# Optimization experiments

Measured on AMD Instinct MI355X. Metric: run time of the kernel, lower is better.

The kernel has to match this reference:

```python
import jax, jax.numpy as jnp
import numpy as np

THRESH = 0.3
DECAY = 0.5


def spike_fn(x):
    # Heaviside threshold (forward only)
    return (x > THRESH).astype(x.dtype)


def setup_inputs() -> dict:
    key = jax.random.key(0)
    k_in, k0, k1, k2 = jax.random.split(key, 4)
    B, D0, T = 128, 512, 512
    inputs = jax.random.uniform(k_in, (B, D0, T), dtype=jnp.float32)
    w0 = jax.random.normal(k0, (512, 1024), dtype=jnp.float32)
    w1 = jax.random.normal(k1, (1024, 1024), dtype=jnp.float32)
    w2 = jax.random.normal(k2, (1024, 512), dtype=jnp.float32)
    return {"inputs": inputs, "w0": w0, "w1": w1, "w2": w2}


def reference(inputs, w0, w1, w2):
    ws = (w0, w1, w2)
    B = inputs.shape[0]
    layer_dims = tuple(w.shape[1] for w in ws)

    # time-major: [T, B, D0]
    xs = jnp.transpose(inputs, (2, 0, 1))

    mem0 = tuple(jnp.zeros((B, d), dtype=inputs.dtype) for d in layer_dims)
    spk0 = tuple(jnp.zeros((B, d), dtype=inputs.dtype) for d in layer_dims)

    def step(carry, x_t):
        mems, spikes = carry
        prev_spike = x_t  # layer-0 spikes come straight from the input
        new_mems, new_spikes = [], []
        for i, w in enumerate(ws):
            # leaky integrate with reset-by-spike, then fire
            mem = mems[i] * DECAY * (1.0 - spikes[i]) + prev_spike @ w
            s = spike_fn(mem)
            new_mems.append(mem)
            new_spikes.append(s)
            prev_spike = s
        return (tuple(new_mems), tuple(new_spikes)), None

    (_, spikes_final), _ = jax.lax.scan(step, (mem0, spk0), xs)
    return spikes_final[-1]
```

## Files before the change

kernel.cpp:

```cpp
#include <hip/hip_runtime.h>


typedef __bf16 bf16;
typedef __attribute__((ext_vector_type(8))) __bf16 bf16x8;
typedef __attribute__((ext_vector_type(16))) float f32x16;
typedef unsigned long long u64;

#define B_   128
#define D0_  512
#define T_   512
#define TS_  128
#define N1_  1024
#define N2_  1024
#define N3_  512
#define MFMA32(a,b,c) __builtin_amdgcn_mfma_f32_32x32x16_bf16((a),(b),(c),0,0,0)

#define GL2LDS(g, l) __builtin_amdgcn_global_load_lds( \
    (const __attribute__((address_space(1))) void*)(g), \
    (__attribute__((address_space(3))) void*)(l), 16, 0, 0)

#define WAIT_BARRIER() do { \
    asm volatile("s_waitcnt vmcnt(0)" ::: "memory"); \
    __builtin_amdgcn_s_barrier(); } while (0)


__global__ __launch_bounds__(256)
void split_w(const float* __restrict__ W, bf16* __restrict__ WTh, bf16* __restrict__ WTl,
             int K, int N)
{
    __shared__ float tile[32][33];
    const int k0 = blockIdx.x * 32, n0 = blockIdx.y * 32;
    const int tx = threadIdx.x & 31, ty = threadIdx.x >> 5;
#pragma unroll
    for (int r = 0; r < 4; ++r)
        tile[ty + r * 8][tx] = W[(size_t)(k0 + ty + r * 8) * N + n0 + tx];
    __syncthreads();
#pragma unroll
    for (int r = 0; r < 4; ++r) {
        int nl = ty + r * 8;
        float v = tile[tx][nl];
        bf16 h = (bf16)v;
        size_t o = (size_t)(n0 + nl) * K + k0 + tx;
        WTh[o] = h;
        WTl[o] = (bf16)(v - (float)h);
    }
}

__global__ __launch_bounds__(64)
void split_wf(const float* __restrict__ W, bf16* __restrict__ Fh, bf16* __restrict__ Fl,
              int K, int N)
{
    const int l = threadIdx.x;
    const int kc = blockIdx.x;
    const int np = blockIdx.y;
    const int c  = np * 32 + (l & 31);
    const int k0 = kc * 16 + (l >> 5) * 8;
    const size_t ob = (((size_t)np * (K / 16) + kc) * 64 + l) * 8;
#pragma unroll
    for (int e = 0; e < 8; ++e) {
        float v = W[(size_t)(k0 + e) * N + c];
        bf16 h = (bf16)v;
        Fh[ob + e] = h;
        Fl[ob + e] = (bf16)(v - (float)h);
    }
}

__global__ __launch_bounds__(256)
void split_x(const float* __restrict__ in, bf16* __restrict__ Xh, bf16* __restrict__ Xl)
{
    __shared__ float tile[32][33];
    const int b = blockIdx.z, d0 = blockIdx.x * 32, t0 = blockIdx.y * 32;
    const int tx = threadIdx.x & 31, ty = threadIdx.x >> 5;
#pragma unroll
    for (int r = 0; r < 4; ++r)
        tile[ty + r * 8][tx] = in[((size_t)b * D0_ + d0 + ty + r * 8) * T_ + t0 + tx];
    __syncthreads();
    const int s = t0 >> 7;
#pragma unroll
    for (int r = 0; r < 4; ++r) {
        int t  = t0 + ty + r * 8;
        int tl = t & (TS_ - 1);
        float v = tile[tx][ty + r * 8];
        bf16 h = (bf16)v;
        size_t o = (((size_t)s * B_ + b) * TS_ + tl) * D0_ + d0 + tx;
        Xh[o] = h;
        Xl[o] = (bf16)(v - (float)h);
    }
}

__device__ __forceinline__ bf16x8 expand8(unsigned v)
{
    union { unsigned u[4]; bf16x8 h; } r;
    const unsigned p = v * 0x8001u;
#pragma unroll
    for (int i = 0; i < 4; ++i)
        r.u[i] = ((p >> (2 * i)) & 0x10001u) * 0x3F80u;
    return r.h;
}

__global__ __launch_bounds__(256, 2)
void snn_layer0(const bf16* __restrict__ Ah, const bf16* __restrict__ Al,
                const bf16* __restrict__ WTh, const bf16* __restrict__ WTl,
                u64* __restrict__ bitsOut)
{
    constexpr int K = D0_;
    __shared__ char smem[65536];
    bf16* sA0  = (bf16*)(smem);
    bf16* sAl0 = (bf16*)(smem + 8192);
    bf16* sB0  = (bf16*)(smem + 16384);
    bf16* sBl0 = (bf16*)(smem + 24576);
    bf16* sA1  = (bf16*)(smem + 32768);
    bf16* sAl1 = (bf16*)(smem + 40960);
    bf16* sB1  = (bf16*)(smem + 49152);
    bf16* sBl1 = (bf16*)(smem + 57344);
    float* If  = (float*)smem;

    const int tid = threadIdx.x, lane = tid & 63, w = tid >> 6;
    const int wm = w & 1, wn = w >> 1;
    const int l31 = lane & 31, kh = lane >> 5;
    const int bid = blockIdx.x;
    const int b  = (bid & 7) | ((bid >> 6) << 3);
    const int nb = ((bid >> 3) & 7) * 128;

    const int i4 = lane >> 2, c4 = lane & 3;
    const int csrc = c4 ^ ((i4 >> 1) & 3);
    const bf16* gBh = WTh + (size_t)(nb + w * 32 + i4) * K + csrc * 8;
    const bf16* gBl = WTl + (size_t)(nb + w * 32 + i4) * K + csrc * 8;
    const int wT = w * 32 * 32;

    int rA[2], rB[2], swA[2], swB[2];
#pragma unroll
    for (int i = 0; i < 2; ++i) {
        rA[i] = wm * 64 + i * 32 + l31;
        rB[i] = wn * 64 + i * 32 + l31;
        swA[i] = (rA[i] >> 1) & 3;
        swB[i] = (rB[i] >> 1) & 3;
    }

    float cm = 0.f, cs = 0.f;
    const int scol = tid & 63;
    float* Ifb = If + (tid >> 6) * 4096;

#define STAGE0(dA, dAl, dBh, dBl, go)                                          \
    do {                                                                       \
        _Pragma("unroll")                                                      \
        for (int inst = 0; inst < 2; ++inst) {                                 \
            GL2LDS(gA  + (size_t)(inst * 16) * K + (go), (dA)  + wT + inst * 16 * 32); \
            GL2LDS(gAl + (size_t)(inst * 16) * K + (go), (dAl) + wT + inst * 16 * 32); \
            GL2LDS(gBh + (size_t)(inst * 16) * K + (go), (dBh) + wT + inst * 16 * 32); \
            GL2LDS(gBl + (size_t)(inst * 16) * K + (go), (dBl) + wT + inst * 16 * 32); \
        }                                                                      \
    } while (0)

#define KSTEP0(cA, cAl, cBh, cBl)                                              \
    do {                                                                       \
        bf16x8 a[2][2], al2[2][2];                                             \
        _Pragma("unroll")                                                      \
        for (int mi = 0; mi < 2; ++mi)                                         \
            _Pragma("unroll")                                                  \
            for (int h = 0; h < 2; ++h) {                                      \
                const int off = rA[mi] * 32 + (((2 * h + kh) ^ swA[mi]) * 8);  \
                a[mi][h]   = *(const bf16x8*)((cA) + off);                     \
                al2[mi][h] = *(const bf16x8*)((cAl) + off);                    \
            }                                                                  \
        _Pragma("unroll")                                                      \
        for (int h = 0; h < 2; ++h) {                                          \
            bf16x8 bh[2], bl[2];                                               \
            _Pragma("unroll")                                                  \
            for (int ni = 0; ni < 2; ++ni) {                                   \
                const int off = rB[ni] * 32 + (((2 * h + kh) ^ swB[ni]) * 8);  \
                bh[ni] = *(const bf16x8*)((cBh) + off);                        \
                bl[ni] = *(const bf16x8*)((cBl) + off);                        \
            }                                                                  \
            _Pragma("unroll")                                                  \
            for (int ni = 0; ni < 2; ++ni)                                     \
                _Pragma("unroll")                                              \
                for (int mi = 0; mi < 2; ++mi)                                 \
                    acc[mi][ni] = MFMA32(a[mi][h], bh[ni], acc[mi][ni]);       \
            _Pragma("unroll")                                                  \
            for (int ni = 0; ni < 2; ++ni)                                     \
                _Pragma("unroll")                                              \
                for (int mi = 0; mi < 2; ++mi)                                 \
                    acc[mi][ni] = MFMA32(al2[mi][h], bh[ni], acc[mi][ni]);     \
            _Pragma("unroll")                                                  \
            for (int ni = 0; ni < 2; ++ni)                                     \
                _Pragma("unroll")                                              \
                for (int mi = 0; mi < 2; ++mi)                                 \
                    acc[mi][ni] = MFMA32(a[mi][h], bl[ni], acc[mi][ni]);       \
        }                                                                      \
        WAIT_BARRIER();                                                        \
    } while (0)

#pragma unroll 1
    for (int s = 0; s < T_ / TS_; ++s) {
        const size_t arow = ((size_t)s * B_ + b) * TS_;
        const bf16* gA  = Ah + (arow + w * 32 + i4) * K + csrc * 8;
        const bf16* gAl = Al + (arow + w * 32 + i4) * K + csrc * 8;

        STAGE0(sA0, sAl0, sB0, sBl0, 0);
        WAIT_BARRIER();

        f32x16 acc[2][2] = {};

#pragma unroll 1
        for (int ks = 0; ks < K / 32; ks += 2) {
            STAGE0(sA1, sAl1, sB1, sBl1, (ks + 1) * 32);
            KSTEP0(sA0, sAl0, sB0, sBl0);
            if (ks + 2 < K / 32)
                STAGE0(sA0, sAl0, sB0, sBl0, (ks + 2) * 32);
            KSTEP0(sA1, sAl1, sB1, sBl1);
        }

        u64 word0 = 0, word1 = 0;
        if (wm == 0) {
#pragma unroll
            for (int ni = 0; ni < 2; ++ni)
#pragma unroll
                for (int mi = 0; mi < 2; ++mi)
#pragma unroll
                    for (int r = 0; r < 16; ++r) {
                        const int tt = mi * 32 + (r & 3) + 8 * (r >> 2) + 4 * kh;
                        If[wn * 4096 + tt * 64 + ni * 32 + l31] = acc[mi][ni][r];
                    }
        }
        __syncthreads();
        if (tid < 128) {
            float m = cm, sp = cs;
#pragma unroll 4
            for (int tt = 0; tt < 64; ++tt) {
                m = m * 0.5f * (1.0f - sp) + Ifb[tt * 64 + scol];
                const bool fire = m > 0.3f;
                sp = fire ? 1.0f : 0.0f;
                u64 bal = __ballot(fire);
                if ((tid & 63) == tt) word0 = bal;
            }
            cm = m; cs = sp;
        }
        __syncthreads();
        if (wm == 1) {
#pragma unroll
            for (int ni = 0; ni < 2; ++ni)
#pragma unroll
                for (int mi = 0; mi < 2; ++mi)
#pragma unroll
                    for (int r = 0; r < 16; ++r) {
                        const int tt = mi * 32 + (r & 3) + 8 * (r >> 2) + 4 * kh;
                        If[wn * 4096 + tt * 64 + ni * 32 + l31] = acc[mi][ni][r];
                    }
        }
        __syncthreads();
        if (tid < 128) {
            float m = cm, sp = cs;
#pragma unroll 4
            for (int tt = 0; tt < 64; ++tt) {
                m = m * 0.5f * (1.0f - sp) + Ifb[tt * 64 + scol];
                const bool fire = m > 0.3f;
                sp = fire ? 1.0f : 0.0f;
                u64 bal = __ballot(fire);
                if ((tid & 63) == tt) word1 = bal;
            }
            cm = m; cs = sp;
            u64* dst = bitsOut + ((size_t)s * B_ + b) * 2048;
            const int j8 = (nb >> 6) + (tid >> 6);
            const int t0 = tid & 63, t1 = 64 + (tid & 63);
            dst[t0 * 16 + (j8 ^ (t0 & 15))] = word0;
            dst[t1 * 16 + (j8 ^ (t1 & 15))] = word1;
        }
        __syncthreads();
    }
#undef STAGE0
#undef KSTEP0
}

template<bool WRITE_BITS>
__global__ __launch_bounds__(256, 2)
void snn_layer_bits(const u64* __restrict__ bitsIn,
                    const bf16* __restrict__ WFh, const bf16* __restrict__ WFl,
                    u64* __restrict__ bitsOut, float* __restrict__ outp, int N)
{
    constexpr int K = 1024, KC = K / 16;
    __shared__ char smem[81920];
    char* bitsLds = smem;
    float* If = (float*)(smem + 16384);

    const int tid = threadIdx.x, lane = tid & 63, w = tid >> 6;
    const int l31 = lane & 31, kh = lane >> 5;
    const int b = blockIdx.y;
    const int nb = blockIdx.x * 128;

    const bf16* wfh = WFh + ((size_t)((nb >> 5) + w) * KC) * 512 + lane * 8;
    const bf16* wfl = WFl + ((size_t)((nb >> 5) + w) * KC) * 512 + lane * 8;

    const int sh8 = 8 * kh;
    const int s15 = l31 & 15;
    int rbase[4];
#pragma unroll
    for (int mi = 0; mi < 4; ++mi)
        rbase[mi] = (mi * 32 + l31) * 128;

    float cm = 0.f, cs = 0.f;

#define CPAIR(cb0, cb1, cb2, cb3)                                              \
    do {                                                                       \
        _Pragma("unroll")                                                      \
        for (int st = 0; st < 2; ++st) {                                       \
            _Pragma("unroll")                                                  \
            for (int h = 0; h < 2; ++h) {                                      \
                const int j = st * 2 + h;                                      \
                bf16x8 a0 = expand8((unsigned)((cb0) >> (32 * st + 16 * h + sh8)) & 0xFFu); \
                bf16x8 a1 = expand8((unsigned)((cb1) >> (32 * st + 16 * h + sh8)) & 0xFFu); \
                bf16x8 a2 = expand8((unsigned)((cb2) >> (32 * st + 16 * h + sh8)) & 0xFFu); \
                bf16x8 a3 = expand8((unsigned)((cb3) >> (32 * st + 16 * h + sh8)) & 0xFFu); \
                __builtin_amdgcn_s_setprio(1);                                 \
                acc[0] = MFMA32(a0, ch[j], acc[0]);                            \
                acc[1] = MFMA32(a1, ch[j], acc[1]);                            \
                acc[2] = MFMA32(a2, ch[j], acc[2]);                            \
                acc[3] = MFMA32(a3, ch[j], acc[3]);                            \
                acc[0] = MFMA32(a0, cl[j], acc[0]);                            \
                acc[1] = MFMA32(a1, cl[j], acc[1]);                            \
                acc[2] = MFMA32(a2, cl[j], acc[2]);                            \
                acc[3] = MFMA32(a3, cl[j], acc[3]);                            \
                __builtin_amdgcn_s_setprio(0);                                 \
            }                                                                  \
        }                                                                      \
    } while (0)

#pragma unroll 1
    for (int s = 0; s < T_ / TS_; ++s) {
        {
            const char* src = (const char*)bitsIn + ((size_t)s * B_ + b) * 16384;
#pragma unroll
            for (int i = 0; i < 4; ++i)
                GL2LDS(src + (w * 4 + i) * 1024 + lane * 16,
                       bitsLds + (w * 4 + i) * 1024);
        }
        WAIT_BARRIER();

        f32x16 acc[4] = {};

        u64 cb0, cb1, cb2, cb3;
        bf16x8 ch[4], cl[4];
        cb0 = *(const u64*)(bitsLds + rbase[0] + ((0 ^ s15) << 3));
        cb1 = *(const u64*)(bitsLds + rbase[1] + ((0 ^ s15) << 3));
        cb2 = *(const u64*)(bitsLds + rbase[2] + ((0 ^ s15) << 3));
        cb3 = *(const u64*)(bitsLds + rbase[3] + ((0 ^ s15) << 3));
#pragma unroll
        for (int j = 0; j < 4; ++j) {
            ch[j] = *(const bf16x8*)(wfh + (size_t)j * 512);
            cl[j] = *(const bf16x8*)(wfl + (size_t)j * 512);
        }

#pragma unroll 1
        for (int pi = 0; pi < 15; ++pi) {
            u64 nb0, nb1, nb2, nb3;
            bf16x8 nh[4], nl[4];
            nb0 = *(const u64*)(bitsLds + rbase[0] + (((pi + 1) ^ s15) << 3));
            nb1 = *(const u64*)(bitsLds + rbase[1] + (((pi + 1) ^ s15) << 3));
            nb2 = *(const u64*)(bitsLds + rbase[2] + (((pi + 1) ^ s15) << 3));
            nb3 = *(const u64*)(bitsLds + rbase[3] + (((pi + 1) ^ s15) << 3));
#pragma unroll
            for (int j = 0; j < 4; ++j) {
                nh[j] = *(const bf16x8*)(wfh + (size_t)((pi + 1) * 4 + j) * 512);
                nl[j] = *(const bf16x8*)(wfl + (size_t)((pi + 1) * 4 + j) * 512);
            }
            CPAIR(cb0, cb1, cb2, cb3);
            cb0 = nb0; cb1 = nb1; cb2 = nb2; cb3 = nb3;
#pragma unroll
            for (int j = 0; j < 4; ++j) { ch[j] = nh[j]; cl[j] = nl[j]; }
        }
        CPAIR(cb0, cb1, cb2, cb3);

#pragma unroll
        for (int mi = 0; mi < 4; ++mi)
#pragma unroll
            for (int r = 0; r < 16; ++r) {
                const int tt = mi * 32 + (r & 3) + 8 * (r >> 2) + 4 * kh;
                If[tt * 128 + w * 32 + l31] = acc[mi][r];
            }
        __syncthreads();
        u64 word0 = 0, word1 = 0;
        if (tid < 128) {
            float m = cm, sp = cs;
#pragma unroll 4
            for (int tt = 0; tt < 128; ++tt) {
                m = m * 0.5f * (1.0f - sp) + If[tt * 128 + tid];
                const bool fire = m > 0.3f;
                sp = fire ? 1.0f : 0.0f;
                if constexpr (WRITE_BITS) {
                    u64 bal = __ballot(fire);
                    if ((tid & 63) == (tt & 63)) {
                        if (tt < 64) word0 = bal; else word1 = bal;
                    }
                }
            }
            cm = m; cs = sp;
            if constexpr (WRITE_BITS) {
                u64* dst = bitsOut + ((size_t)s * B_ + b) * 2048;
                const int j8 = (nb >> 6) + (tid >> 6);
                const int t0 = tid & 63, t1 = 64 + (tid & 63);
                dst[t0 * 16 + (j8 ^ (t0 & 15))] = word0;
                dst[t1 * 16 + (j8 ^ (t1 & 15))] = word1;
            } else {
                if (s == T_ / TS_ - 1)
                    outp[(size_t)b * N + nb + tid] = cs;
            }
        }
    }
#undef CPAIR
}

extern "C" void kernel_launch(void* const* d_in, const int* in_sizes, int n_in,
                              void* d_out, int out_size, void* d_ws, size_t ws_size,
                              hipStream_t stream)
{
    const float* x  = (const float*)d_in[0];
    const float* w0 = (const float*)d_in[1];
    const float* w1 = (const float*)d_in[2];
    const float* w2 = (const float*)d_in[3];
    float* out = (float*)d_out;

    char* p = (char*)d_ws;
    bf16* w0h  = (bf16*)p; p += (size_t)N1_ * D0_ * 2;
    bf16* w0l  = (bf16*)p; p += (size_t)N1_ * D0_ * 2;
    bf16* wf1h = (bf16*)p; p += (size_t)N2_ * N1_ * 2;
    bf16* wf1l = (bf16*)p; p += (size_t)N2_ * N1_ * 2;
    bf16* wf2h = (bf16*)p; p += (size_t)N3_ * N2_ * 2;
    bf16* wf2l = (bf16*)p; p += (size_t)N3_ * N2_ * 2;
    bf16* Xh   = (bf16*)p; p += (size_t)T_ * B_ * D0_ * 2;
    bf16* Xl   = (bf16*)p; p += (size_t)T_ * B_ * D0_ * 2;
    u64* bits0 = (u64*)p;  p += (size_t)(T_/TS_) * B_ * TS_ * (N1_/8);
    u64* bits1 = (u64*)p;  p += (size_t)(T_/TS_) * B_ * TS_ * (N2_/8);

    split_w<<<dim3(D0_/32, N1_/32), 256, 0, stream>>>(w0, w0h, w0l, D0_, N1_);
    split_wf<<<dim3(N1_/16, N2_/32), 64, 0, stream>>>(w1, wf1h, wf1l, N1_, N2_);
    split_wf<<<dim3(N2_/16, N3_/32), 64, 0, stream>>>(w2, wf2h, wf2l, N2_, N3_);
    split_x<<<dim3(D0_/32, T_/32, B_), 256, 0, stream>>>(x, Xh, Xl);

    snn_layer0<<<dim3(B_ * (N1_/128)), 256, 0, stream>>>(Xh, Xl, w0h, w0l, bits0);
    snn_layer_bits<true ><<<dim3(N2_/128, B_), 256, 0, stream>>>(
        bits0, wf1h, wf1l, bits1, nullptr, N2_);
    snn_layer_bits<false><<<dim3(N3_/128, B_), 256, 0, stream>>>(
        bits1, wf2h, wf2l, nullptr, out, N3_);
}
```

Measured before the change: 831.9 us.

## Retile layer kernel into 2x2 warp grid with rolling weight prefetch and halved LDS

Each of the four warps in snn_layer_bits now computes a 64x64 output tile (2x2 MFMA accumulators) instead of a 128x32 tile. This halves the bit-word loads per warp and lets each weight fragment feed two row blocks. The weight prefetch becomes a rolling 4-slot register ring, interleaved with the MFMA steps. The If staging buffer shrinks to 32KB, so the two time halves are written and scanned in two phases with extra barriers. The aim is better register reuse and lower LDS use per block, possibly raising occupancy, at the cost of more synchronisation and a serialized two-phase membrane scan.

```diff
diff --git a/kernel.cpp b/kernel.cpp
--- a/kernel.cpp
+++ b/kernel.cpp
@@ -279,50 +279,51 @@
                     u64* __restrict__ bitsOut, float* __restrict__ outp, int N)
 {
     constexpr int K = 1024, KC = K / 16;
-    __shared__ char smem[81920];
+    __shared__ char smem[49152];
     char* bitsLds = smem;
     float* If = (float*)(smem + 16384);
 
     const int tid = threadIdx.x, lane = tid & 63, w = tid >> 6;
+    const int wm = w & 1, wn = w >> 1;
     const int l31 = lane & 31, kh = lane >> 5;
     const int b = blockIdx.y;
     const int nb = blockIdx.x * 128;
 
-    const bf16* wfh = WFh + ((size_t)((nb >> 5) + w) * KC) * 512 + lane * 8;
-    const bf16* wfl = WFl + ((size_t)((nb >> 5) + w) * KC) * 512 + lane * 8;
-
-    const int sh8 = 8 * kh;
-    const int s15 = l31 & 15;
-    int rbase[4];
-#pragma unroll
-    for (int mi = 0; mi < 4; ++mi)
-        rbase[mi] = (mi * 32 + l31) * 128;
+    const size_t fb0 = ((size_t)((nb >> 5) + wn * 2) * KC) * 512 + (size_t)lane * 8;
+    const size_t fb1 = fb0 + (size_t)KC * 512;
+    const bf16* h0 = WFh + fb0;
+    const bf16* h1 = WFh + fb1;
+    const bf16* l0 = WFl + fb0;
+    const bf16* l1 = WFl + fb1;
+
+    const int sh8 = 8 * kh, s15 = l31 & 15;
+    const int rA0b = (wm * 64 + l31) * 128;
+    const int rA1b = (wm * 64 + 32 + l31) * 128;
 
     float cm = 0.f, cs = 0.f;
-
-#define CPAIR(cb0, cb1, cb2, cb3)                                              \
+    const int scol = tid & 63;
+    float* Ifb = If + (tid >> 6) * 4096;
+
+#define LOADQ(sl, kc)                                                          \
     do {                                                                       \
-        _Pragma("unroll")                                                      \
-        for (int st = 0; st < 2; ++st) {                                       \
-            _Pragma("unroll")                                                  \
-            for (int h = 0; h < 2; ++h) {                                      \
-                const int j = st * 2 + h;                                      \
-                bf16x8 a0 = expand8((unsigned)((cb0) >> (32 * st + 16 * h + sh8)) & 0xFFu); \
-                bf16x8 a1 = expand8((unsigned)((cb1) >> (32 * st + 16 * h + sh8)) & 0xFFu); \
-                bf16x8 a2 = expand8((unsigned)((cb2) >> (32 * st + 16 * h + sh8)) & 0xFFu); \
-                bf16x8 a3 = expand8((unsigned)((cb3) >> (32 * st + 16 * h + sh8)) & 0xFFu); \
-                __builtin_amdgcn_s_setprio(1);                                 \
-                acc[0] = MFMA32(a0, ch[j], acc[0]);                            \
-                acc[1] = MFMA32(a1, ch[j], acc[1]);                            \
-                acc[2] = MFMA32(a2, ch[j], acc[2]);                            \
-                acc[3] = MFMA32(a3, ch[j], acc[3]);                            \
-                acc[0] = MFMA32(a0, cl[j], acc[0]);                            \
-                acc[1] = MFMA32(a1, cl[j], acc[1]);                            \
-                acc[2] = MFMA32(a2, cl[j], acc[2]);                            \
-                acc[3] = MFMA32(a3, cl[j], acc[3]);                            \
-                __builtin_amdgcn_s_setprio(0);                                 \
-            }                                                                  \
-        }                                                                      \
+        q0h[sl] = *(const bf16x8*)(h0 + (size_t)(kc) * 512);                   \
+        q1h[sl] = *(const bf16x8*)(h1 + (size_t)(kc) * 512);                   \
+        q0l[sl] = *(const bf16x8*)(l0 + (size_t)(kc) * 512);                   \
+        q1l[sl] = *(const bf16x8*)(l1 + (size_t)(kc) * 512);                   \
+    } while (0)
+
+#define JSTEP(j, CB0, CB1)                                                     \
+    do {                                                                       \
+        bf16x8 a0 = expand8((unsigned)((CB0) >> (16 * (j) + sh8)) & 0xFFu);    \
+        bf16x8 a1 = expand8((unsigned)((CB1) >> (16 * (j) + sh8)) & 0xFFu);    \
+        acc[0][0] = MFMA32(a0, q0h[j], acc[0][0]);                             \
+        acc[1][0] = MFMA32(a1, q0h[j], acc[1][0]);                             \
+        acc[0][1] = MFMA32(a0, q1h[j], acc[0][1]);                             \
+        acc[1][1] = MFMA32(a1, q1h[j], acc[1][1]);                             \
+        acc[0][0] = MFMA32(a0, q0l[j], acc[0][0]);                             \
+        acc[1][0] = MFMA32(a1, q0l[j], acc[1][0]);                             \
+        acc[0][1] = MFMA32(a0, q1l[j], acc[0][1]);                             \
+        acc[1][1] = MFMA32(a1, q1l[j], acc[1][1]);                             \
     } while (0)
 
 #pragma unroll 1
@@ -336,61 +337,80 @@
         }
         WAIT_BARRIER();
 
-        f32x16 acc[4] = {};
-
-        u64 cb0, cb1, cb2, cb3;
-        bf16x8 ch[4], cl[4];
-        cb0 = *(const u64*)(bitsLds + rbase[0] + ((0 ^ s15) << 3));
-        cb1 = *(const u64*)(bitsLds + rbase[1] + ((0 ^ s15) << 3));
-        cb2 = *(const u64*)(bitsLds + rbase[2] + ((0 ^ s15) << 3));
-        cb3 = *(const u64*)(bitsLds + rbase[3] + ((0 ^ s15) << 3));
-#pragma unroll
-        for (int j = 0; j < 4; ++j) {
-            ch[j] = *(const bf16x8*)(wfh + (size_t)j * 512);
-            cl[j] = *(const bf16x8*)(wfl + (size_t)j * 512);
-        }
+        f32x16 acc[2][2] = {};
+        bf16x8 q0h[4], q0l[4], q1h[4], q1l[4];
+
+        LOADQ(0, 0);
+        LOADQ(1, 1);
+        u64 cb0 = *(const u64*)(bitsLds + rA0b + ((0 ^ s15) << 3));
+        u64 cb1 = *(const u64*)(bitsLds + rA1b + ((0 ^ s15) << 3));
 
 #pragma unroll 1
         for (int pi = 0; pi < 15; ++pi) {
-            u64 nb0, nb1, nb2, nb3;
-            bf16x8 nh[4], nl[4];
-            nb0 = *(const u64*)(bitsLds + rbase[0] + (((pi + 1) ^ s15) << 3));
-            nb1 = *(const u64*)(bitsLds + rbase[1] + (((pi + 1) ^ s15) << 3));
-            nb2 = *(const u64*)(bitsLds + rbase[2] + (((pi + 1) ^ s15) << 3));
-            nb3 = *(const u64*)(bitsLds + rbase[3] + (((pi + 1) ^ s15) << 3));
-#pragma unroll
-            for (int j = 0; j < 4; ++j) {
-                nh[j] = *(const bf16x8*)(wfh + (size_t)((pi + 1) * 4 + j) * 512);
-                nl[j] = *(const bf16x8*)(wfl + (size_t)((pi + 1) * 4 + j) * 512);
-            }
-            CPAIR(cb0, cb1, cb2, cb3);
-            cb0 = nb0; cb1 = nb1; cb2 = nb2; cb3 = nb3;
-#pragma unroll
-            for (int j = 0; j < 4; ++j) { ch[j] = nh[j]; cl[j] = nl[j]; }
-        }
-        CPAIR(cb0, cb1, cb2, cb3);
-
-#pragma unroll
-        for (int mi = 0; mi < 4; ++mi)
-#pragma unroll
-            for (int r = 0; r < 16; ++r) {
-                const int tt = mi * 32 + (r & 3) + 8 * (r >> 2) + 4 * kh;
-                If[tt * 128 + w * 32 + l31] = acc[mi][r];
-            }
-        __syncthreads();
+            const u64 nb0 = *(const u64*)(bitsLds + rA0b + (((pi + 1) ^ s15) << 3));
+            const u64 nb1 = *(const u64*)(bitsLds + rA1b + (((pi + 1) ^ s15) << 3));
+            const int kc = pi * 4;
+            LOADQ(2, kc + 2); JSTEP(0, cb0, cb1);
+            LOADQ(3, kc + 3); JSTEP(1, cb0, cb1);
+            LOADQ(0, kc + 4); JSTEP(2, cb0, cb1);
+            LOADQ(1, kc + 5); JSTEP(3, cb0, cb1);
+            cb0 = nb0; cb1 = nb1;
+        }
+        LOADQ(2, 62); JSTEP(0, cb0, cb1);
+        LOADQ(3, 63); JSTEP(1, cb0, cb1);
+        JSTEP(2, cb0, cb1);
+        JSTEP(3, cb0, cb1);
+
         u64 word0 = 0, word1 = 0;
+        if (wm == 0) {
+#pragma unroll
+            for (int ni = 0; ni < 2; ++ni)
+#pragma unroll
+                for (int mi = 0; mi < 2; ++mi)
+#pragma unroll
+                    for (int r = 0; r < 16; ++r) {
+                        const int tt = mi * 32 + (r & 3) + 8 * (r >> 2) + 4 * kh;
+                        If[wn * 4096 + tt * 64 + ni * 32 + l31] = acc[mi][ni][r];
+                    }
+        }
+        __syncthreads();
         if (tid < 128) {
             float m = cm, sp = cs;
 #pragma unroll 4
-            for (int tt = 0; tt < 128; ++tt) {
-                m = m * 0.5f * (1.0f - sp) + If[tt * 128 + tid];
+            for (int tt = 0; tt < 64; ++tt) {
+                m = m * 0.5f * (1.0f - sp) + Ifb[tt * 64 + scol];
                 const bool fire = m > 0.3f;
                 sp = fire ? 1.0f : 0.0f;
                 if constexpr (WRITE_BITS) {
                     u64 bal = __ballot(fire);
-                    if ((tid & 63) == (tt & 63)) {
-                        if (tt < 64) word0 = bal; else word1 = bal;
+                    if ((tid & 63) == tt) word0 = bal;
+                }
+            }
+            cm = m; cs = sp;
+        }
+        __syncthreads();
+        if (wm == 1) {
+#pragma unroll
+            for (int ni = 0; ni < 2; ++ni)
+#pragma unroll
+                for (int mi = 0; mi < 2; ++mi)
+#pragma unroll
+                    for (int r = 0; r < 16; ++r) {
+                        const int tt = mi * 32 + (r & 3) + 8 * (r >> 2) + 4 * kh;
+                        If[wn * 4096 + tt * 64 + ni * 32 + l31] = acc[mi][ni][r];
                     }
+        }
+        __syncthreads();
+        if (tid < 128) {
+            float m = cm, sp = cs;
+#pragma unroll 4
+            for (int tt = 0; tt < 64; ++tt) {
+                m = m * 0.5f * (1.0f - sp) + Ifb[tt * 64 + scol];
+                const bool fire = m > 0.3f;
+                sp = fire ? 1.0f : 0.0f;
+                if constexpr (WRITE_BITS) {
+                    u64 bal = __ballot(fire);
+                    if ((tid & 63) == tt) word1 = bal;
                 }
             }
             cm = m; cs = sp;
@@ -405,8 +425,10 @@
                     outp[(size_t)b * N + nb + tid] = cs;
             }
         }
-    }
-#undef CPAIR
+        __syncthreads();
+    }
+#undef LOADQ
+#undef JSTEP
 }
 
 extern "C" void kernel_launch(void* const* d_in, const int* in_sizes, int n_in,
```

Result: faster. 806.0 us (-3.1%).
